# Kernel optimization log

Hardware: AMD Instinct MI355X
Metric: run time of the kernel (lower is better)

## Reference

```python
import jax, jax.numpy as jnp
import numpy as np

LEVELS = [2, 3, 4, 5, 6]
IMG = 1024
BATCH = 8
NUM_ANCHORS = 3
PRE_NMS_TOP_K = 2000
NUM_PROPOSALS = 1000
NMS_IOU = 0.7
BBOX_XFORM_CLIP = float(np.log(1000.0 / 16.0))


def _make_anchors(level):
    stride = 2 ** level
    fs = IMG // stride
    base = 4.0 * stride
    aspects = np.array([0.5, 1.0, 2.0], np.float32)
    hs = base * np.sqrt(aspects)
    ws = base / np.sqrt(aspects)
    cy = (np.arange(fs, dtype=np.float32) + 0.5) * stride
    cx = (np.arange(fs, dtype=np.float32) + 0.5) * stride
    yy, xx = np.meshgrid(cy, cx, indexing='ij')
    yy = yy[:, :, None]
    xx = xx[:, :, None]
    # [fs, fs, A, 4] in (ymin, xmin, ymax, xmax)
    boxes = np.stack([yy - hs / 2, xx - ws / 2, yy + hs / 2, xx + ws / 2], axis=-1)
    return boxes.reshape(fs * fs * NUM_ANCHORS, 4).astype(np.float32)


def setup_inputs():
    key = jax.random.key(0)
    inp = {}
    for i, lvl in enumerate(LEVELS):
        fs = IMG // (2 ** lvl)
        kb, ks = jax.random.split(jax.random.fold_in(key, i))
        inp['boxes_l%d' % lvl] = jax.random.normal(kb, (BATCH, fs, fs, NUM_ANCHORS * 4), jnp.float32) * 0.2
        inp['scores_l%d' % lvl] = jax.random.normal(ks, (BATCH, fs, fs, NUM_ANCHORS), jnp.float32)
        anc = jnp.asarray(_make_anchors(lvl))
        inp['anchors_l%d' % lvl] = jnp.tile(anc[None], (BATCH, 1, 1))
    inp['image_shape'] = jnp.full((BATCH, 2), float(IMG), jnp.float32)
    return inp


def decode_boxes(encoded, anchors):
    dy, dx, dh, dw = jnp.split(encoded, 4, axis=-1)
    dh = jnp.minimum(dh, BBOX_XFORM_CLIP)
    dw = jnp.minimum(dw, BBOX_XFORM_CLIP)
    ay0, ax0, ay1, ax1 = jnp.split(anchors, 4, axis=-1)
    ah = ay1 - ay0
    aw = ax1 - ax0
    ayc = ay0 + 0.5 * ah
    axc = ax0 + 0.5 * aw
    yc = dy * ah + ayc
    xc = dx * aw + axc
    h = jnp.exp(dh) * ah
    w = jnp.exp(dw) * aw
    return jnp.concatenate([yc - 0.5 * h, xc - 0.5 * w, yc + 0.5 * h, xc + 0.5 * w], axis=-1)


def clip_boxes(boxes, image_shape):
    # image_shape: [B, 1, 2] (h, w) -> max coords (h, w, h, w)
    maxes = jnp.concatenate([image_shape, image_shape], axis=-1)
    return jnp.clip(boxes, 0.0, maxes)


def top_k_boxes(boxes, scores, k):
    scores_k, idx = jax.lax.top_k(scores, k)
    boxes_k = jnp.take_along_axis(boxes, idx[..., None], axis=1)
    return boxes_k, scores_k


def sorted_nms_padded(scores, boxes, max_output_size, iou_threshold):
    # scores [B,K] sorted descending, boxes [B,K,4]. Greedy NMS.
    B, K = scores.shape
    areas = (boxes[..., 2] - boxes[..., 0]) * (boxes[..., 3] - boxes[..., 1])  # [B,K]
    idxs = jnp.arange(K)

    def step(kept, i):
        bi = jax.lax.dynamic_slice_in_dim(boxes, i, 1, axis=1)  # [B,1,4]
        ai = jax.lax.dynamic_slice_in_dim(areas, i, 1, axis=1)  # [B,1]
        ki = jax.lax.dynamic_slice_in_dim(kept, i, 1, axis=1)   # [B,1]
        iy = jnp.maximum(0.0, jnp.minimum(bi[..., 2], boxes[..., 2]) - jnp.maximum(bi[..., 0], boxes[..., 0]))
        ix = jnp.maximum(0.0, jnp.minimum(bi[..., 3], boxes[..., 3]) - jnp.maximum(bi[..., 1], boxes[..., 1]))
        inter = iy * ix  # [B,K]
        iou = inter / (ai + areas - inter + 1e-8)
        suppress = (iou > iou_threshold) & (idxs[None, :] > i) & ki
        return kept & (~suppress), None

    kept0 = jnp.ones((B, K), dtype=bool)
    kept, _ = jax.lax.scan(step, kept0, idxs)
    out_scores = jnp.where(kept, scores, 0.0)
    out_boxes = boxes * kept[..., None].astype(boxes.dtype)
    b_out, s_out = top_k_boxes(out_boxes, out_scores, max_output_size)
    return s_out, b_out


def _multi_level_rois(raw_boxes, raw_scores, anchors, image_shape):
    img = image_shape[:, None, :]  # [B,1,2]
    rois, roi_scores = [], []
    for rb, rs, ab in zip(raw_boxes, raw_scores, anchors):
        B, fh, fw, na = rs.shape
        nb = fh * fw * na
        sc = jax.nn.sigmoid(rs.reshape(B, nb))
        bx = rb.reshape(B, nb, 4)
        bx = decode_boxes(bx, ab)
        bx = clip_boxes(bx, img)
        pre_k = min(nb, PRE_NMS_TOP_K)
        post_k = min(nb, NUM_PROPOSALS)
        bx, sc = top_k_boxes(bx, sc, pre_k)
        s_out, b_out = sorted_nms_padded(sc, bx, post_k, NMS_IOU)
        rois.append(b_out)
        roi_scores.append(s_out)
    all_rois = jnp.concatenate(rois, axis=1)
    all_scores = jnp.concatenate(roi_scores, axis=1)
    k = min(all_scores.shape[1], NUM_PROPOSALS)
    sel_rois, sel_scores = top_k_boxes(all_rois, all_scores, k)
    return sel_rois, sel_scores


def reference(boxes_l2, boxes_l3, boxes_l4, boxes_l5, boxes_l6,
              scores_l2, scores_l3, scores_l4, scores_l5, scores_l6,
              anchors_l2, anchors_l3, anchors_l4, anchors_l5, anchors_l6,
              image_shape):
    raw_boxes = [boxes_l2, boxes_l3, boxes_l4, boxes_l5, boxes_l6]
    raw_scores = [scores_l2, scores_l3, scores_l4, scores_l5, scores_l6]
    anchors = [anchors_l2, anchors_l3, anchors_l4, anchors_l5, anchors_l6]
    return _multi_level_rois(raw_boxes, raw_scores, anchors, image_shape)
```

## Files before the change

### kernel.cpp

```cpp
#include <hip/hip_runtime.h>
#include <hip/hip_bf16.h>
#include <cstdint>

constexpr int BATCH = 8;
constexpr int NL = 5;
constexpr int CNTS[5] = {196608, 49152, 12288, 3072, 768};
constexpr int LOFF[5] = {0, 196608, 245760, 258048, 261120};
constexpr int PERB  = 261888;
constexpr int TOTC  = BATCH * PERB;
constexpr int PREK[5]  = {2000, 2000, 2000, 2000, 768};
constexpr int POSTK[5] = {1000, 1000, 1000, 1000, 768};
constexpr int COFF[5]  = {0, 1000, 2000, 3000, 4000};
constexpr int CONCATN  = 4768;
constexpr int SELSTRIDE = 2048;
constexpr int CANDCAP   = 8192;
constexpr int NREP      = 64;
constexpr int REPCAP    = 512;
constexpr int NBINS     = 16384;
constexpr int MASKROWS  = 2000;
constexpr int MASKW     = 32;
constexpr int SCH       = 128;
constexpr int ROWS_PER_BATCH = 4 * 2000 + 768;
constexpr float IOU_THR = 0.7f;
constexpr float CLIPV = 4.135166556742356f;
constexpr double TAU = 23488103.0 / 33554432.0;

struct Ptrs {
    const float* bx[5];
    const float* sc[5];
    const float* an[5];
    const float* img;
};

__device__ __forceinline__ unsigned long long readlane_u64(unsigned long long v, int src) {
    unsigned int lo = (unsigned int)v;
    unsigned int hi = (unsigned int)(v >> 32);
    lo = (unsigned int)__builtin_amdgcn_readlane((int)lo, src);
    hi = (unsigned int)__builtin_amdgcn_readlane((int)hi, src);
    return ((unsigned long long)hi << 32) | lo;
}

__global__ __launch_bounds__(1024) void k_hist(Ptrs p, unsigned int* __restrict__ hist) {
#pragma clang fp contract(off)
    __shared__ unsigned int h2[NBINS / 2];
    constexpr int CLI[11] = {0, 0, 0, 0, 0, 0, 1, 1, 2, 3, 4};
    constexpr int COF[11] = {0, 32768, 65536, 98304, 131072, 163840, 0, 24576, 0, 0, 0};
    constexpr int CLN[11] = {32768, 32768, 32768, 32768, 32768, 32768, 24576, 24576, 12288, 3072, 768};
    int blk = blockIdx.x;
    int b = blk / 11, c = blk % 11;
    int li = CLI[c], off = COF[c], len = CLN[c];
    int tid = threadIdx.x;
    for (int i = tid; i < NBINS / 2; i += 1024) h2[i] = 0;
    __syncthreads();
    const float* sp = p.sc[li] + (size_t)b * CNTS[li] + off;
    for (int i = tid; i < len; i += 1024) {
        float s = sp[i];
        float sig = 1.0f / (1.0f + expf(-s));
        unsigned int bin = __float_as_uint(sig) >> 16;
        atomicAdd(&h2[bin >> 1], 1u << ((bin & 1) << 4));
    }
    __syncthreads();
    unsigned int* H = hist + (size_t)(b * NL + li) * NBINS;
    for (int i = tid; i < NBINS / 2; i += 1024) {
        unsigned int v = h2[i];
        if (v & 0xFFFFu) atomicAdd(&H[2 * i], v & 0xFFFFu);
        if (v >> 16) atomicAdd(&H[2 * i + 1], v >> 16);
    }
}

__global__ void k_findbin(const unsigned int* __restrict__ hist, int* __restrict__ T) {
    int bl = blockIdx.x;
    int li = bl % NL;
    unsigned int K = (unsigned int)PREK[li];
    __shared__ unsigned int csum[256];
    const unsigned int* h = hist + (size_t)bl * NBINS;
    int tid = threadIdx.x;
    unsigned int s = 0;
    for (int k = 0; k < 64; ++k) s += h[tid * 64 + k];
    csum[tid] = s;
    __syncthreads();
    if (tid == 0) {
        unsigned int cum = 0;
        int t = 0;
        for (int c = 255; c >= 0; --c) {
            if (cum + csum[c] >= K) {
                for (int bin = c * 64 + 63; bin >= c * 64; --bin) {
                    cum += h[bin];
                    if (cum >= K) { t = bin; break; }
                }
                break;
            }
            cum += csum[c];
        }
        T[bl] = t;
    }
}

__global__ void k_compact(Ptrs p, const int* __restrict__ T,
                          unsigned long long* __restrict__ cand, unsigned int* __restrict__ cntR) {
#pragma clang fp contract(off)
    int g = blockIdx.x * blockDim.x + threadIdx.x;
    if (g >= TOTC) return;
    int b = g / PERB;
    int r = g - b * PERB;
    int li;
    if      (r < LOFF[1]) li = 0;
    else if (r < LOFF[2]) li = 1;
    else if (r < LOFF[3]) li = 2;
    else if (r < LOFF[4]) li = 3;
    else                  li = 4;
    int i = r - LOFF[li];
    int bl = b * NL + li;
    int rep = blockIdx.x & (NREP - 1);

    float s = p.sc[li][(size_t)b * CNTS[li] + i];
    float sig = 1.0f / (1.0f + expf(-s));
    unsigned int bits = __float_as_uint(sig);
    bool pass = ((int)(bits >> 16) >= T[bl]);
    unsigned long long ball = __ballot(pass);
    int lane = threadIdx.x & 63;
    unsigned int base = 0;
    if (lane == 0 && ball != 0ull)
        base = atomicAdd(&cntR[rep * 64 + bl], (unsigned int)__popcll(ball));
    base = __shfl((int)base, 0);
    if (pass) {
        unsigned int pos = base + (unsigned int)__popcll(ball & ((1ull << lane) - 1ull));
        if (pos < REPCAP)
            cand[((size_t)bl * NREP + rep) * REPCAP + pos] =
                ((unsigned long long)bits << 32) | (unsigned long long)(0xFFFFFFFFu - (unsigned int)i);
    }
}

template <int NH>
__device__ __forceinline__ void rank_emit(const unsigned long long* keys, int n, int K, int tid,
                                          const float4* bxp, const float4* anp,
                                          float hmax, float wmax,
                                          float* sels_o, float4* selb_o, float* selA_o) {
#pragma clang fp contract(off)
    unsigned long long myk[NH];
    int rnk[NH];
#pragma unroll
    for (int h = 0; h < NH; ++h) {
        int idx = tid + h * 1024;
        myk[h] = (idx < n) ? keys[idx] : ~0ull;
        rnk[h] = 0;
    }
    int j = 0;
    for (; j + 4 <= n; j += 4) {
        unsigned long long k0 = keys[j], k1 = keys[j + 1], k2 = keys[j + 2], k3 = keys[j + 3];
#pragma unroll
        for (int h = 0; h < NH; ++h)
            rnk[h] += (int)(k0 > myk[h]) + (int)(k1 > myk[h]) +
                      (int)(k2 > myk[h]) + (int)(k3 > myk[h]);
    }
    for (; j < n; ++j) {
        unsigned long long kj = keys[j];
#pragma unroll
        for (int h = 0; h < NH; ++h) rnk[h] += (int)(kj > myk[h]);
    }
#pragma unroll
    for (int h = 0; h < NH; ++h) {
        int idx = tid + h * 1024;
        int r = rnk[h];
        if (idx < n && r < K) {
            unsigned long long kk = myk[h];
            unsigned int gi = 0xFFFFFFFFu - (unsigned int)(kk & 0xFFFFFFFFull);
            const float4 e = bxp[gi];
            const float4 a = anp[gi];
            float dy = e.x, dx = e.y;
            float dh = fminf(e.z, CLIPV), dw = fminf(e.w, CLIPV);
            float ah = a.z - a.x, aw = a.w - a.y;
            float ayc = a.x + 0.5f * ah, axc = a.y + 0.5f * aw;
            float yc = dy * ah + ayc, xc = dx * aw + axc;
            float hh = expf(dh) * ah, ww = expf(dw) * aw;
            float y0 = yc - 0.5f * hh, x0 = xc - 0.5f * ww;
            float y1 = yc + 0.5f * hh, x1 = xc + 0.5f * ww;
            y0 = fminf(fmaxf(y0, 0.f), hmax);
            x0 = fminf(fmaxf(x0, 0.f), wmax);
            y1 = fminf(fmaxf(y1, 0.f), hmax);
            x1 = fminf(fmaxf(x1, 0.f), wmax);
            sels_o[r] = __uint_as_float((unsigned int)(kk >> 32));
            selb_o[r] = make_float4(y0, x0, y1, x1);
            selA_o[r] = (y1 - y0) * (x1 - x0);
        }
    }
}

__global__ __launch_bounds__(1024) void k_sortsel(const unsigned long long* __restrict__ cand,
                                                  const unsigned int* __restrict__ cntR, Ptrs p,
                                                  float4* __restrict__ selb, float* __restrict__ sels,
                                                  float* __restrict__ selA) {
    __shared__ unsigned long long keys[CANDCAP];
    __shared__ int pref[NREP + 1];
    int bl = blockIdx.x;
    int tid = threadIdx.x;
    int b = bl / NL, li = bl % NL;
    int K = PREK[li];
    if (tid == 0) {
        int run = 0;
        for (int rp = 0; rp < NREP; ++rp) {
            pref[rp] = run;
            int c = min((int)cntR[rp * 64 + bl], REPCAP);
            if (run + c > CANDCAP) c = CANDCAP - run;
            run += c;
        }
        pref[NREP] = run;
    }
    __syncthreads();
    int n = pref[NREP];
    for (int rp = 0; rp < NREP; ++rp) {
        int base = pref[rp], c = pref[rp + 1] - pref[rp];
        const unsigned long long* src = cand + ((size_t)bl * NREP + rp) * REPCAP;
        for (int j = tid; j < c; j += 1024) keys[base + j] = src[j];
    }
    __syncthreads();

    int nn = CNTS[li];
    float hmax = p.img[b * 2 + 0];
    float wmax = p.img[b * 2 + 1];
    const float4* bxp = reinterpret_cast<const float4*>(p.bx[li]) + (size_t)b * nn;
    const float4* anp = reinterpret_cast<const float4*>(p.an[li]) + (size_t)b * nn;
    float* so = sels + (size_t)bl * SELSTRIDE;
    float4* bo = selb + (size_t)bl * SELSTRIDE;
    float* ao = selA + (size_t)bl * SELSTRIDE;
    int nh = (n + 1023) >> 10;
    if (nh <= 2)      rank_emit<2>(keys, n, K, tid, bxp, anp, hmax, wmax, so, bo, ao);
    else if (nh <= 4) rank_emit<4>(keys, n, K, tid, bxp, anp, hmax, wmax, so, bo, ao);
    else              rank_emit<8>(keys, n, K, tid, bxp, anp, hmax, wmax, so, bo, ao);
}

__global__ void k_mask(const float4* __restrict__ selb, const float* __restrict__ selA,
                       unsigned long long* __restrict__ mask) {
#pragma clang fp contract(off)
    int rg = blockIdx.x;
    int b = rg / ROWS_PER_BATCH;
    int rem = rg - b * ROWS_PER_BATCH;
    int li, i;
    if (rem < 8000) { li = rem / 2000; i = rem - li * 2000; }
    else            { li = 4; i = rem - 8000; }
    int bl = b * NL + li;
    int K = PREK[li];
    const float4* bb = selb + (size_t)bl * SELSTRIDE;
    const float* aA = selA + (size_t)bl * SELSTRIDE;
    float4 bi = bb[i];
    float ai = aA[i];
    int tid = threadIdx.x;
    unsigned long long* mrow = mask + ((size_t)bl * MASKROWS + i) * MASKW;
    for (int cb = (i >> 6) << 6; cb < K; cb += 256) {
        int c = cb + tid;
        bool sup = false;
        if (c > i && c < K) {
            float4 bj = bb[c];
            float aj = aA[c];
            float iy = fmaxf(0.f, fminf(bi.z, bj.z) - fmaxf(bi.x, bj.x));
            float ix = fmaxf(0.f, fminf(bi.w, bj.w) - fmaxf(bi.y, bj.y));
            float inter = iy * ix;
            float aden = ai + aj - inter + 1e-8f;
            sup = ((double)inter >= TAU * (double)aden);
        }
        unsigned long long bal = __ballot(sup);
        int wb = cb + (tid & ~63);
        if ((tid & 63) == 0 && wb < K) mrow[wb >> 6] = bal;
    }
}

__global__ __launch_bounds__(256) void k_scan(const unsigned long long* __restrict__ mask,
                                              unsigned long long* __restrict__ kept) {
    __shared__ unsigned long long lbuf[2][SCH * MASKW];
    __shared__ int stopflag;
    int bl = blockIdx.x;
    int li = bl % NL;
    int K = PREK[li];
    int W = (K + 63) >> 6;
    int PK = POSTK[li];
    int tid = threadIdx.x;
    int lane = tid & 63;
    int wv = tid >> 6;
    const unsigned long long* m = mask + (size_t)bl * MASKROWS * MASKW;
    int nchunks = (K + SCH - 1) / SCH;

    auto load_chunk = [&](int c, int t0, int nt) {
        int rbase = c * SCH;
        int nrows = min(SCH, K - rbase);
        int nu2 = nrows * (MASKW / 2);
        const ulonglong2* src = reinterpret_cast<const ulonglong2*>(m + (size_t)rbase * MASKW);
        ulonglong2* dst = reinterpret_cast<ulonglong2*>(lbuf[c & 1]);
        if (tid >= t0)
            for (int j = tid - t0; j < nu2; j += nt) dst[j] = src[j];
    };

    if (tid == 0) stopflag = 0;
    load_chunk(0, 0, 256);
    __syncthreads();

    unsigned long long removed = 0, local = 0;
    int keptcnt = 0;
    for (int c = 0; c < nchunks; ++c) {
        if (c + 1 < nchunks) load_chunk(c + 1, 64, 192);
        if (wv == 0) {
            const unsigned long long* ch = lbuf[c & 1];
            int rbase = c * SCH;
            int nrows = min(SCH, K - rbase);

            unsigned long long rvA[8], rgA[8], rvB[8], rgB[8];
            auto loadw = [&](unsigned long long (&rv)[8], unsigned long long (&rg)[8], int w0) {
                int g = (rbase + w0) >> 6;
#pragma unroll
                for (int k2 = 0; k2 < 8; ++k2) {
                    rv[k2] = ch[(w0 + k2) * MASKW + (lane & (MASKW - 1))];
                    rg[k2] = ch[(w0 + k2) * MASKW + g];
                }
            };
            auto procw = [&](unsigned long long (&rv)[8], unsigned long long (&rg)[8], int w0) {
                int ii0 = rbase + w0;
                int g = ii0 >> 6;
                if ((ii0 & 63) == 0) local = readlane_u64(removed, g);
                unsigned long long gemask = (lane >= g) ? ~0ull : 0ull;
#pragma unroll
                for (int k2 = 0; k2 < 8; ++k2) {
                    bool keptb = ((local >> ((ii0 & 63) + k2)) & 1ull) == 0ull;
                    unsigned long long sel = keptb ? ~0ull : 0ull;
                    removed |= rv[k2] & sel & gemask;
                    local |= rg[k2] & sel;
                    keptcnt += keptb ? 1 : 0;
                }
            };

            loadw(rvA, rgA, 0);
            for (int w0 = 0; w0 < nrows; w0 += 16) {
                if (w0 + 8 < nrows) loadw(rvB, rgB, w0 + 8);
                procw(rvA, rgA, w0);
                if (w0 + 8 < nrows) {
                    if (w0 + 16 < nrows) loadw(rvA, rgA, w0 + 16);
                    procw(rvB, rgB, w0 + 8);
                }
            }
            if (keptcnt >= PK && c + 1 < nchunks) {
                if (lane >= (c + 1) * (SCH / 64)) removed = ~0ull;
                if (lane == 0) stopflag = 1;
            }
        }
        __syncthreads();
        if (stopflag) break;
    }
    if (wv == 0 && lane < W) {
        int remn = K - lane * 64;
        unsigned long long valid = (remn >= 64) ? ~0ull : ((1ull << remn) - 1ull);
        kept[bl * MASKW + lane] = (~removed) & valid;
    }
}

__global__ void k_lvlout(const unsigned long long* __restrict__ kept,
                         const float* __restrict__ sels, const float4* __restrict__ selb,
                         float* __restrict__ cscores, float4* __restrict__ cboxes) {
    int bl = blockIdx.x;
    int b = bl / NL, li = bl % NL;
    int K = PREK[li];
    int W = (K + 63) >> 6;
    int PK = POSTK[li];
    int tid = threadIdx.x;
    __shared__ unsigned long long kw[32];
    __shared__ int pref[33];
    if (tid < W) kw[tid] = kept[bl * MASKW + tid];
    __syncthreads();
    if (tid == 0) {
        int run = 0;
        for (int w = 0; w < W; ++w) { pref[w] = run; run += __popcll(kw[w]); }
        pref[W] = run;
    }
    __syncthreads();
    int total = pref[W];
    int nused = min(total, PK);
    float* cs = cscores + (size_t)b * CONCATN + COFF[li];
    float4* cbx = cboxes + (size_t)b * CONCATN + COFF[li];
    if (tid < W) {
        int rank = pref[tid];
        unsigned long long w64 = kw[tid];
        while (w64 != 0ull && rank < PK) {
            int j = __ffsll(w64) - 1;
            w64 &= (w64 - 1);
            int pidx = tid * 64 + j;
            cs[rank] = sels[(size_t)bl * SELSTRIDE + pidx];
            cbx[rank] = selb[(size_t)bl * SELSTRIDE + pidx];
            ++rank;
        }
    }
    for (int r = nused + tid; r < PK; r += 256) {
        cs[r] = 0.f;
        cbx[r] = make_float4(0.f, 0.f, 0.f, 0.f);
    }
}

__global__ __launch_bounds__(1024) void k_final(const float* __restrict__ cscores,
                                                const float4* __restrict__ cboxes,
                                                float* __restrict__ out) {
    __shared__ unsigned long long keys[CONCATN];
    int b = blockIdx.x;
    int tid = threadIdx.x;
    const float* cs = cscores + (size_t)b * CONCATN;
    for (int i = tid; i < CONCATN; i += 1024)
        keys[i] = (((unsigned long long)__float_as_uint(cs[i]) << 32) |
                   (unsigned long long)(0xFFFFFFFFu - (unsigned int)i));
    __syncthreads();
    const float4* cbx = cboxes + (size_t)b * CONCATN;
    float4* ob = reinterpret_cast<float4*>(out) + (size_t)b * 1000;
    float* os = out + (size_t)BATCH * 1000 * 4 + (size_t)b * 1000;
    for (int i = tid; i < CONCATN; i += 1024) {
        unsigned long long k = keys[i];
        int myli = min(i / 1000, 4);
        int rank = i - COFF[myli];
#pragma unroll
        for (int r = 0; r < NL; ++r) {
            if (r == myli) continue;
            const unsigned long long* run = keys + COFF[r];
            int lo = 0, hi = POSTK[r];
            while (lo < hi) {
                int mid = (lo + hi) >> 1;
                if (run[mid] > k) lo = mid + 1; else hi = mid;
            }
            rank += lo;
        }
        if (rank < 1000) {
            ob[rank] = cbx[i];
            os[rank] = __uint_as_float((unsigned int)(k >> 32));
        }
    }
}

extern "C" void kernel_launch(void* const* d_in, const int* in_sizes, int n_in,
                              void* d_out, int out_size, void* d_ws, size_t ws_size,
                              hipStream_t stream) {
    Ptrs p;
    bool dict_order = (in_sizes[2] == 6291456);
    for (int l = 0; l < 5; ++l) {
        if (dict_order) {
            p.bx[l] = (const float*)d_in[3 * l + 0];
            p.sc[l] = (const float*)d_in[3 * l + 1];
            p.an[l] = (const float*)d_in[3 * l + 2];
        } else {
            p.bx[l] = (const float*)d_in[l];
            p.sc[l] = (const float*)d_in[5 + l];
            p.an[l] = (const float*)d_in[10 + l];
        }
    }
    p.img = (const float*)d_in[15];

    char* ws = (char*)d_ws;
    size_t off = 0;
    auto walloc = [&](size_t sz) -> void* {
        void* r = ws + off;
        off = (off + sz + 255) & ~(size_t)255;
        return r;
    };
    unsigned int* hist         = (unsigned int*)walloc((size_t)40 * NBINS * 4);
    unsigned int* cntR         = (unsigned int*)walloc((size_t)NREP * 64 * 4);
    int* T                     = (int*)walloc(40 * 4);
    unsigned long long* cand   = (unsigned long long*)walloc((size_t)40 * NREP * REPCAP * 8);
    float4* selb               = (float4*)walloc((size_t)40 * SELSTRIDE * 16);
    float* sels                = (float*)walloc((size_t)40 * SELSTRIDE * 4);
    float* selA                = (float*)walloc((size_t)40 * SELSTRIDE * 4);
    unsigned long long* mask   = (unsigned long long*)walloc((size_t)40 * MASKROWS * MASKW * 8);
    unsigned long long* kept   = (unsigned long long*)walloc((size_t)40 * MASKW * 8);
    float* cscores             = (float*)walloc((size_t)BATCH * CONCATN * 4);
    float4* cboxes             = (float4*)walloc((size_t)BATCH * CONCATN * 16);
    (void)ws_size;

    hipMemsetAsync(hist, 0, (size_t)40 * NBINS * 4, stream);
    hipMemsetAsync(cntR, 0, (size_t)NREP * 64 * 4, stream);

    k_hist<<<BATCH * 11, 1024, 0, stream>>>(p, hist);
    k_findbin<<<40, 256, 0, stream>>>(hist, T);
    k_compact<<<(TOTC + 255) / 256, 256, 0, stream>>>(p, T, cand, cntR);
    k_sortsel<<<40, 1024, 0, stream>>>(cand, cntR, p, selb, sels, selA);
    k_mask<<<BATCH * ROWS_PER_BATCH, 256, 0, stream>>>(selb, selA, mask);
    k_scan<<<40, 256, 0, stream>>>(mask, kept);
    k_lvlout<<<40, 256, 0, stream>>>(kept, sels, selb, cscores, cboxes);
    k_final<<<8, 1024, 0, stream>>>(cscores, cboxes, (float*)d_out);
}
```

Baseline: 493.0 us.

## Split rank-select into gather kernel and multi-block rank kernel using lane broadcasts

The single 40-block rank-and-emit kernel, which staged candidates in shared memory, is replaced by two kernels. A gather kernel compacts the candidates into a dense global buffer padded to a multiple of 64. A rank kernel then spreads each (batch, level) over 12 blocks of 256 threads. Each wave reads 64 keys at a time from global memory and broadcasts them with readlane instead of shared-memory reads. This uses many more CUs for the O(n²) ranking, at the cost of an extra launch, a global round trip, and a serial tail when n exceeds 12*256.

```diff
diff --git a/kernel.cpp b/kernel.cpp
--- a/kernel.cpp
+++ b/kernel.cpp
@@ -17,6 +17,7 @@
 constexpr int NREP      = 64;
 constexpr int REPCAP    = 512;
 constexpr int NBINS     = 16384;
+constexpr int NSUB      = 12;
 constexpr int MASKROWS  = 2000;
 constexpr int MASKW     = 32;
 constexpr int SCH       = 128;
@@ -131,39 +132,75 @@
     }
 }
 
-template <int NH>
-__device__ __forceinline__ void rank_emit(const unsigned long long* keys, int n, int K, int tid,
-                                          const float4* bxp, const float4* anp,
-                                          float hmax, float wmax,
-                                          float* sels_o, float4* selb_o, float* selA_o) {
+__global__ __launch_bounds__(256) void k_gather(const unsigned long long* __restrict__ cand,
+                                                const unsigned int* __restrict__ cntR,
+                                                unsigned long long* __restrict__ dense,
+                                                int* __restrict__ nArr) {
+    __shared__ int pref[NREP + 1];
+    int bl = blockIdx.x;
+    int tid = threadIdx.x;
+    if (tid == 0) {
+        int run = 0;
+        for (int rp = 0; rp < NREP; ++rp) {
+            pref[rp] = run;
+            int c = min((int)cntR[rp * 64 + bl], REPCAP);
+            if (run + c > CANDCAP) c = CANDCAP - run;
+            run += c;
+        }
+        pref[NREP] = run;
+        nArr[bl] = run;
+    }
+    __syncthreads();
+    int n = pref[NREP];
+    unsigned long long* d = dense + (size_t)bl * CANDCAP;
+    for (int rp = 0; rp < NREP; ++rp) {
+        int base = pref[rp], c = pref[rp + 1] - pref[rp];
+        const unsigned long long* src = cand + ((size_t)bl * NREP + rp) * REPCAP;
+        for (int j = tid; j < c; j += 256) d[base + j] = src[j];
+    }
+    int npad = (n + 63) & ~63;
+    for (int j = n + tid; j < npad; j += 256) d[j] = 0ull;
+}
+
+__global__ __launch_bounds__(256) void k_rank(const unsigned long long* __restrict__ dense,
+                                              const int* __restrict__ nArr, Ptrs p,
+                                              float4* __restrict__ selb, float* __restrict__ sels,
+                                              float* __restrict__ selA) {
 #pragma clang fp contract(off)
-    unsigned long long myk[NH];
-    int rnk[NH];
-#pragma unroll
-    for (int h = 0; h < NH; ++h) {
-        int idx = tid + h * 1024;
-        myk[h] = (idx < n) ? keys[idx] : ~0ull;
-        rnk[h] = 0;
-    }
-    int j = 0;
-    for (; j + 4 <= n; j += 4) {
-        unsigned long long k0 = keys[j], k1 = keys[j + 1], k2 = keys[j + 2], k3 = keys[j + 3];
-#pragma unroll
-        for (int h = 0; h < NH; ++h)
-            rnk[h] += (int)(k0 > myk[h]) + (int)(k1 > myk[h]) +
-                      (int)(k2 > myk[h]) + (int)(k3 > myk[h]);
-    }
-    for (; j < n; ++j) {
-        unsigned long long kj = keys[j];
-#pragma unroll
-        for (int h = 0; h < NH; ++h) rnk[h] += (int)(kj > myk[h]);
-    }
-#pragma unroll
-    for (int h = 0; h < NH; ++h) {
-        int idx = tid + h * 1024;
-        int r = rnk[h];
-        if (idx < n && r < K) {
-            unsigned long long kk = myk[h];
+    int blk = blockIdx.x;
+    int bl = blk / NSUB, s = blk % NSUB;
+    int b = bl / NL, li = bl % NL;
+    int K = PREK[li];
+    int tid = threadIdx.x, lane = tid & 63;
+    int n = nArr[bl];
+    const unsigned long long* d = dense + (size_t)bl * CANDCAP;
+    int nt = (n + 63) >> 6;
+
+    int nn = CNTS[li];
+    float hmax = p.img[b * 2 + 0];
+    float wmax = p.img[b * 2 + 1];
+    const float4* bxp = reinterpret_cast<const float4*>(p.bx[li]) + (size_t)b * nn;
+    const float4* anp = reinterpret_cast<const float4*>(p.an[li]) + (size_t)b * nn;
+    float* so = sels + (size_t)bl * SELSTRIDE;
+    float4* bo = selb + (size_t)bl * SELSTRIDE;
+    float* ao = selA + (size_t)bl * SELSTRIDE;
+
+    auto process = [&](int idx) {
+        unsigned long long myk = (idx < n) ? d[idx] : ~0ull;
+        int rnk = 0;
+        const unsigned long long* g = d + lane;
+        unsigned long long cur = (nt > 0) ? g[0] : 0ull, nxt = 0ull;
+        for (int t = 0; t < nt; ++t) {
+            if (t + 1 < nt) nxt = g[(size_t)(t + 1) * 64];
+#pragma unroll 16
+            for (int j = 0; j < 64; ++j) {
+                unsigned long long bc = readlane_u64(cur, j);
+                rnk += (int)(bc > myk);
+            }
+            cur = nxt;
+        }
+        if (idx < n && rnk < K) {
+            unsigned long long kk = myk;
             unsigned int gi = 0xFFFFFFFFu - (unsigned int)(kk & 0xFFFFFFFFull);
             const float4 e = bxp[gi];
             const float4 a = anp[gi];
@@ -179,54 +216,15 @@
             x0 = fminf(fmaxf(x0, 0.f), wmax);
             y1 = fminf(fmaxf(y1, 0.f), hmax);
             x1 = fminf(fmaxf(x1, 0.f), wmax);
-            sels_o[r] = __uint_as_float((unsigned int)(kk >> 32));
-            selb_o[r] = make_float4(y0, x0, y1, x1);
-            selA_o[r] = (y1 - y0) * (x1 - x0);
-        }
-    }
-}
-
-__global__ __launch_bounds__(1024) void k_sortsel(const unsigned long long* __restrict__ cand,
-                                                  const unsigned int* __restrict__ cntR, Ptrs p,
-                                                  float4* __restrict__ selb, float* __restrict__ sels,
-                                                  float* __restrict__ selA) {
-    __shared__ unsigned long long keys[CANDCAP];
-    __shared__ int pref[NREP + 1];
-    int bl = blockIdx.x;
-    int tid = threadIdx.x;
-    int b = bl / NL, li = bl % NL;
-    int K = PREK[li];
-    if (tid == 0) {
-        int run = 0;
-        for (int rp = 0; rp < NREP; ++rp) {
-            pref[rp] = run;
-            int c = min((int)cntR[rp * 64 + bl], REPCAP);
-            if (run + c > CANDCAP) c = CANDCAP - run;
-            run += c;
-        }
-        pref[NREP] = run;
-    }
-    __syncthreads();
-    int n = pref[NREP];
-    for (int rp = 0; rp < NREP; ++rp) {
-        int base = pref[rp], c = pref[rp + 1] - pref[rp];
-        const unsigned long long* src = cand + ((size_t)bl * NREP + rp) * REPCAP;
-        for (int j = tid; j < c; j += 1024) keys[base + j] = src[j];
-    }
-    __syncthreads();
-
-    int nn = CNTS[li];
-    float hmax = p.img[b * 2 + 0];
-    float wmax = p.img[b * 2 + 1];
-    const float4* bxp = reinterpret_cast<const float4*>(p.bx[li]) + (size_t)b * nn;
-    const float4* anp = reinterpret_cast<const float4*>(p.an[li]) + (size_t)b * nn;
-    float* so = sels + (size_t)bl * SELSTRIDE;
-    float4* bo = selb + (size_t)bl * SELSTRIDE;
-    float* ao = selA + (size_t)bl * SELSTRIDE;
-    int nh = (n + 1023) >> 10;
-    if (nh <= 2)      rank_emit<2>(keys, n, K, tid, bxp, anp, hmax, wmax, so, bo, ao);
-    else if (nh <= 4) rank_emit<4>(keys, n, K, tid, bxp, anp, hmax, wmax, so, bo, ao);
-    else              rank_emit<8>(keys, n, K, tid, bxp, anp, hmax, wmax, so, bo, ao);
+            so[rnk] = __uint_as_float((unsigned int)(kk >> 32));
+            bo[rnk] = make_float4(y0, x0, y1, x1);
+            ao[rnk] = (y1 - y0) * (x1 - x0);
+        }
+    };
+
+    process(s * 256 + tid);
+    if (s == NSUB - 1)
+        for (int b2 = NSUB * 256; b2 < n; b2 += 256) process(b2 + tid);
 }
 
 __global__ void k_mask(const float4* __restrict__ selb, const float* __restrict__ selA,
@@ -456,6 +454,8 @@
     unsigned int* cntR         = (unsigned int*)walloc((size_t)NREP * 64 * 4);
     int* T                     = (int*)walloc(40 * 4);
     unsigned long long* cand   = (unsigned long long*)walloc((size_t)40 * NREP * REPCAP * 8);
+    unsigned long long* dense  = (unsigned long long*)walloc((size_t)40 * CANDCAP * 8);
+    int* nArr                  = (int*)walloc(40 * 4);
     float4* selb               = (float4*)walloc((size_t)40 * SELSTRIDE * 16);
     float* sels                = (float*)walloc((size_t)40 * SELSTRIDE * 4);
     float* selA                = (float*)walloc((size_t)40 * SELSTRIDE * 4);
@@ -471,7 +471,8 @@
     k_hist<<<BATCH * 11, 1024, 0, stream>>>(p, hist);
     k_findbin<<<40, 256, 0, stream>>>(hist, T);
     k_compact<<<(TOTC + 255) / 256, 256, 0, stream>>>(p, T, cand, cntR);
-    k_sortsel<<<40, 1024, 0, stream>>>(cand, cntR, p, selb, sels, selA);
+    k_gather<<<40, 256, 0, stream>>>(cand, cntR, dense, nArr);
+    k_rank<<<40 * NSUB, 256, 0, stream>>>(dense, nArr, p, selb, sels, selA);
     k_mask<<<BATCH * ROWS_PER_BATCH, 256, 0, stream>>>(selb, selA, mask);
     k_scan<<<40, 256, 0, stream>>>(mask, kept);
     k_lvlout<<<40, 256, 0, stream>>>(kept, sels, selb, cscores, cboxes);
```

After: 420.3 us. -14.7%, faster.
